# Kernel optimization log

Measured on AMD Instinct MI355X. Metric: run time of the kernel, lower is better.

## Reference

```python
import jax, jax.numpy as jnp
import numpy as np

B, L, H, V = 2048, 1024, 64, 64
LN_EPS = 1e-5
DELTA_EPS = 1e-6


def setup_inputs() -> dict:
    key = jax.random.key(0)
    ks = jax.random.split(key, 16)
    s = 0.05
    return {
        'seq': jax.random.randint(ks[0], (B, L), 0, V),
        'embed_W': jax.random.normal(ks[1], (V, H), jnp.float32),
        'ff_w1': jax.random.normal(ks[2], (H, 2 * H), jnp.float32) * s,
        'ff_b1': jnp.zeros((2 * H,), jnp.float32),
        'ff_w2': jax.random.normal(ks[3], (2 * H, H), jnp.float32) * s,
        'ff_b2': jnp.zeros((H,), jnp.float32),
        'ln_g': jnp.ones((H,), jnp.float32),
        'ln_b': jnp.zeros((H,), jnp.float32),
        'gate_w1': jax.random.normal(ks[4], (H, 16), jnp.float32) * s,
        'gate_b1': jnp.zeros((16,), jnp.float32),
        'gate_w2': jax.random.normal(ks[5], (16, 1), jnp.float32) * s,
        'gate_b2': jnp.zeros((1,), jnp.float32),
        'read_w': jax.random.normal(ks[6], (H, H), jnp.float32) * s,
        'read_b': jnp.zeros((H,), jnp.float32),
        'out_w': jax.random.normal(ks[7], (H, V), jnp.float32) * s,
        'out_b': jnp.zeros((V,), jnp.float32),
    }


def _layernorm(x, g, b):
    mu = jnp.mean(x, axis=-1, keepdims=True)
    var = jnp.var(x, axis=-1, keepdims=True)
    return (x - mu) * jax.lax.rsqrt(var + LN_EPS) * g + b


def reference(seq, embed_W, ff_w1, ff_b1, ff_w2, ff_b2, ln_g, ln_b,
              gate_w1, gate_b1, gate_w2, gate_b2, read_w, read_b, out_w, out_b):
    h = embed_W[seq]                                        # (B, L, H)
    ff = jnp.maximum(h @ ff_w1 + ff_b1, 0.0) @ ff_w2 + ff_b2
    h = _layernorm(h + ff, ln_g, ln_b)                      # (B, L, H)

    ks_seq = jnp.transpose(h[:, :-1, :], (1, 0, 2))         # (L-1, B, H) keys for scan

    def step(M, k):
        # k: (B, H); M: (B, H, H) fast-weight memory
        g = jax.nn.sigmoid(jnp.maximum(k @ gate_w1 + gate_b1, 0.0) @ gate_w2 + gate_b2)  # (B, 1)
        v_pred = jnp.einsum('bij,bj->bi', jax.lax.stop_gradient(M), k)
        denom = jnp.sum(k * k, axis=-1, keepdims=True) + DELTA_EPS
        dv = k - v_pred / denom                             # (B, H)
        dM = dv[:, :, None] * k[:, None, :]                 # outer product (B, H, H)
        return M + g[:, :, None] * dM, None

    M0 = jnp.zeros((h.shape[0], H, H), h.dtype)
    M, _ = jax.lax.scan(step, M0, ks_seq)

    q = h[:, -1, :]
    ctx = jnp.einsum('bij,bj->bi', M, q)                    # (B, H)
    logits = (ctx @ read_w + read_b) @ out_w + out_b        # (B, V)
    return logits
```

## Files before the change

### kernel.cpp

```cpp
#include <hip/hip_runtime.h>
#include <math.h>

#define Bsz 2048
#define Lsz 1024
#define SW  8

#define OFF_G   0
#define OFF_GC  4096
#define OFF_P   8192
#define OFF_WC  12288
#define OFF_GV  16384
#define OFF_C   16448
#define OFF_BC  16512

__device__ __forceinline__ float __rlf(float v, int i) {
    return __int_as_float(__builtin_amdgcn_readlane(__float_as_int(v), i));
}

__global__ __launch_bounds__(128) void prep1_kernel(
    const float* __restrict__ embed_W, const float* __restrict__ ff_w1, const float* __restrict__ ff_b1,
    const float* __restrict__ ff_w2, const float* __restrict__ ff_b2, const float* __restrict__ ln_g,
    const float* __restrict__ ln_b, const float* __restrict__ gate_w1, const float* __restrict__ gate_b1,
    const float* __restrict__ gate_w2, const float* __restrict__ gate_b2, const float* __restrict__ read_w,
    const float* __restrict__ read_b, const float* __restrict__ out_w, const float* __restrict__ out_b,
    float* __restrict__ ws)
{
    const int tid = threadIdx.x;
    const int blk = blockIdx.x;
    if (blk < 64) {
        const int v = blk;
        __shared__ float z[128];
        __shared__ float hsh[64];
        const float* Ev = embed_W + (v << 6);
        float a = ff_b1[tid];
        #pragma unroll
        for (int i = 0; i < 64; ++i) a = fmaf(Ev[i], ff_w1[i * 128 + tid], a);
        z[tid] = fmaxf(a, 0.0f);
        __syncthreads();
        if (tid < 64) {
            float x = Ev[tid] + ff_b2[tid];
            #pragma unroll
            for (int j = 0; j < 128; ++j) x = fmaf(z[j], ff_w2[j * 64 + tid], x);
            float mu = x;
            #pragma unroll
            for (int off = 32; off > 0; off >>= 1) mu += __shfl_xor(mu, off);
            mu *= (1.0f / 64.0f);
            const float dd = x - mu;
            float var = dd * dd;
            #pragma unroll
            for (int off = 32; off > 0; off >>= 1) var += __shfl_xor(var, off);
            var *= (1.0f / 64.0f);
            const float rstd = rsqrtf(var + 1e-5f);
            const float hv = fmaf(dd * rstd, ln_g[tid], ln_b[tid]);
            hsh[tid] = hv;
            float dn = hv * hv;
            #pragma unroll
            for (int off = 32; off > 0; off >>= 1) dn += __shfl_xor(dn, off);
            dn += 1e-6f;
            float a2 = 0.0f;
            if (tid < 16) {
                float um = gate_b1[tid];
                #pragma unroll
                for (int i = 0; i < 64; ++i) um = fmaf(hsh[i], gate_w1[i * 16 + tid], um);
                a2 = fmaxf(um, 0.0f) * gate_w2[tid];
            }
            #pragma unroll
            for (int off = 8; off > 0; off >>= 1) a2 += __shfl_xor(a2, off);
            ws[OFF_G + (v << 6) + tid] = hv;
            if (tid == 0) {
                a2 += gate_b2[0];
                const float g = 1.0f / (1.0f + expf(-a2));
                ws[OFF_GV + v] = g;
                ws[OFF_C + v]  = g / dn;
            }
        }
    } else if (blk < 128) {
        const int j = blk - 64;
        if (tid < 64) {
            float a = 0.0f;
            #pragma unroll
            for (int m = 0; m < 64; ++m) a = fmaf(read_w[(j << 6) + m], out_w[(m << 6) + tid], a);
            ws[OFF_WC + (j << 6) + tid] = a;
        }
    } else {
        if (tid < 64) {
            float a = out_b[tid];
            #pragma unroll
            for (int jj = 0; jj < 64; ++jj) a = fmaf(read_b[jj], out_w[(jj << 6) + tid], a);
            ws[OFF_BC + tid] = a;
        }
    }
}

__global__ __launch_bounds__(64) void prep2_kernel(float* __restrict__ ws)
{
    const int tid = threadIdx.x;
    const int blk = blockIdx.x;
    __shared__ float tT[65 * 64];
    for (int idx = tid; idx < 4096; idx += 64) {
        const int w = idx >> 6, j = idx & 63;
        tT[j * 65 + w] = ws[OFF_G + idx];
    }
    __syncthreads();
    if (blk < 64) {
        const int v = blk;
        const float cv = ws[OFF_C + v];
        float a = 0.0f;
        #pragma unroll
        for (int j = 0; j < 64; ++j) a = fmaf(tT[j * 65 + v], tT[j * 65 + tid], a);
        ws[OFF_G  + (v << 6) + tid] = a;
        ws[OFF_GC + (v << 6) + tid] = cv * a;
    } else {
        const int v = blk - 64;
        const float gv = ws[OFF_GV + v];
        float a = 0.0f;
        #pragma unroll
        for (int j = 0; j < 64; ++j)
            a = fmaf(tT[j * 65 + v], ws[OFF_WC + (j << 6) + tid], a);
        ws[OFF_P + (v << 6) + tid] = gv * a;
    }
}

__global__ __launch_bounds__(SW * 64) void scan_kernel(const int* __restrict__ seq,
                                                       const float* __restrict__ ws,
                                                       float* __restrict__ out)
{
    __shared__ float2 ldsGP[65 * 64];
    __shared__ int    pk[SW][16 + 256 + 64];
    __shared__ float  ldsbc[64];

    const int tid  = threadIdx.x;
    const int wave = tid >> 6;
    const int lane = tid & 63;

    {
        const float4* srcGc = (const float4*)(ws + OFF_GC);
        const float4* srcP  = (const float4*)(ws + OFF_P);
        for (int i = tid; i < 1024; i += SW * 64) {
            const float4 g4 = srcGc[i];
            const float4 p4 = srcP[i];
            const int base = i << 2;
            ldsGP[base + 0] = make_float2(g4.x, p4.x);
            ldsGP[base + 1] = make_float2(g4.y, p4.y);
            ldsGP[base + 2] = make_float2(g4.z, p4.z);
            ldsGP[base + 3] = make_float2(g4.w, p4.w);
        }
    }
    if (tid < 64) {
        ldsGP[4096 + tid] = make_float2(0.0f, 0.0f);
        ldsbc[tid] = ws[OFF_BC + tid];
    }
    const int b = blockIdx.x * SW + wave;
    int* P = pk[wave] + 16;
    {
        const int4* src = (const int4*)(seq + (size_t)b * Lsz);
        #pragma unroll
        for (int i = 0; i < 4; ++i) {
            const int4 tv = src[i * 64 + lane];
            P[i * 64 + lane] = tv.x | (tv.y << 8) | (tv.z << 16) | (tv.w << 24);
        }
        if (lane < 16) pk[wave][lane] = 0x40404040;
    }
    __syncthreads();

    const int lastw = P[255];
    const int tokL  = (lastw >> 24) & 0xFF;
    if (lane == 0) P[255] = (lastw & 0x00FFFFFF) | (64 << 24);

    float D   = ws[OFF_G + (tokL << 6) + lane];
    float acc = ldsbc[lane];

    int    tkA[16], tkB[16];
    float2 gpA[16], gpB[16];

    int tokv = P[248 + lane];
    #pragma unroll
    for (int j = 0; j < 4; ++j) {
        const int w = __builtin_amdgcn_readlane(tokv, 7 - j);
        tkA[4 * j + 0] = (w >> 24) & 0xFF;
        tkA[4 * j + 1] = (w >> 16) & 0xFF;
        tkA[4 * j + 2] = (w >>  8) & 0xFF;
        tkA[4 * j + 3] =  w        & 0xFF;
    }
    #pragma unroll
    for (int k = 0; k < 16; ++k) gpA[k] = ldsGP[(tkA[k] << 6) + lane];
    #pragma unroll
    for (int j = 0; j < 4; ++j) {
        const int w = __builtin_amdgcn_readlane(tokv, 3 - j);
        tkB[4 * j + 0] = (w >> 24) & 0xFF;
        tkB[4 * j + 1] = (w >> 16) & 0xFF;
        tkB[4 * j + 2] = (w >>  8) & 0xFF;
        tkB[4 * j + 3] =  w        & 0xFF;
    }
    #pragma unroll
    for (int k = 0; k < 16; ++k) gpB[k] = ldsGP[(tkB[k] << 6) + lane];

    for (int n = 0; n < 32; ++n) {
        const int tokvN = P[240 - 8 * n + lane];
        __builtin_amdgcn_s_setprio(1);
        #pragma unroll
        for (int k = 0; k < 16; ++k) {
            const float d = __rlf(D, tkA[k]);
            D   = fmaf(-d, gpA[k].x, D);
            acc = fmaf( d, gpA[k].y, acc);
        }
        __builtin_amdgcn_s_setprio(0);
        #pragma unroll
        for (int j = 0; j < 4; ++j) {
            const int w = __builtin_amdgcn_readlane(tokvN, 7 - j);
            tkA[4 * j + 0] = (w >> 24) & 0xFF;
            tkA[4 * j + 1] = (w >> 16) & 0xFF;
            tkA[4 * j + 2] = (w >>  8) & 0xFF;
            tkA[4 * j + 3] =  w        & 0xFF;
        }
        #pragma unroll
        for (int k = 0; k < 16; ++k) gpA[k] = ldsGP[(tkA[k] << 6) + lane];
        __builtin_amdgcn_s_setprio(1);
        #pragma unroll
        for (int k = 0; k < 16; ++k) {
            const float d = __rlf(D, tkB[k]);
            D   = fmaf(-d, gpB[k].x, D);
            acc = fmaf( d, gpB[k].y, acc);
        }
        __builtin_amdgcn_s_setprio(0);
        #pragma unroll
        for (int j = 0; j < 4; ++j) {
            const int w = __builtin_amdgcn_readlane(tokvN, 3 - j);
            tkB[4 * j + 0] = (w >> 24) & 0xFF;
            tkB[4 * j + 1] = (w >> 16) & 0xFF;
            tkB[4 * j + 2] = (w >>  8) & 0xFF;
            tkB[4 * j + 3] =  w        & 0xFF;
        }
        #pragma unroll
        for (int k = 0; k < 16; ++k) gpB[k] = ldsGP[(tkB[k] << 6) + lane];
    }

    out[(size_t)b * 64 + lane] = acc;
}

extern "C" void kernel_launch(void* const* d_in, const int* in_sizes, int n_in,
                              void* d_out, int out_size, void* d_ws, size_t ws_size,
                              hipStream_t stream) {
    const int*   seq     = (const int*)  d_in[0];
    const float* embed_W = (const float*)d_in[1];
    const float* ff_w1   = (const float*)d_in[2];
    const float* ff_b1   = (const float*)d_in[3];
    const float* ff_w2   = (const float*)d_in[4];
    const float* ff_b2   = (const float*)d_in[5];
    const float* ln_g    = (const float*)d_in[6];
    const float* ln_b    = (const float*)d_in[7];
    const float* gate_w1 = (const float*)d_in[8];
    const float* gate_b1 = (const float*)d_in[9];
    const float* gate_w2 = (const float*)d_in[10];
    const float* gate_b2 = (const float*)d_in[11];
    const float* read_w  = (const float*)d_in[12];
    const float* read_b  = (const float*)d_in[13];
    const float* out_w   = (const float*)d_in[14];
    const float* out_b   = (const float*)d_in[15];
    float* ws  = (float*)d_ws;
    float* out = (float*)d_out;

    hipLaunchKernelGGL(prep1_kernel, dim3(129), dim3(128), 0, stream,
                       embed_W, ff_w1, ff_b1, ff_w2, ff_b2, ln_g, ln_b,
                       gate_w1, gate_b1, gate_w2, gate_b2, read_w, read_b,
                       out_w, out_b, ws);
    hipLaunchKernelGGL(prep2_kernel, dim3(128), dim3(64), 0, stream, ws);
    hipLaunchKernelGGL(scan_kernel, dim3(Bsz / SW), dim3(SW * 64), 0, stream,
                       seq, ws, out);
}
```

Baseline: 121.5 us.

## Block the serial scan recurrence into 4-step triangular solves to shorten dependency chain

Replaces the strictly sequential per-token update (readlane of D, then two FMAs) with blocks of four tokens. For each block, all four D values are read up front, a small lower-triangular system is solved using cross-token Gram entries fetched via readlane, and then D and acc are updated. This is meant to shorten the serial readlane-to-FMA dependency chain, which limits latency in a single-wave scan. The cost is more readlanes and FMAs per token, plus some floating-point reassociation.

```diff
diff --git a/kernel.cpp b/kernel.cpp
--- a/kernel.cpp
+++ b/kernel.cpp
@@ -121,6 +121,37 @@
     }
 }
 
+#define SUB4(tk, gp, q)                                                          \
+  {                                                                              \
+    const int   t0 = tk[4*(q)+0], t1 = tk[4*(q)+1], t2 = tk[4*(q)+2], t3 = tk[4*(q)+3]; \
+    const float2 g0 = gp[4*(q)+0], g1 = gp[4*(q)+1], g2 = gp[4*(q)+2], g3 = gp[4*(q)+3]; \
+    const float M10 = __rlf(g0.x, t1);                                           \
+    const float M20 = __rlf(g0.x, t2);                                           \
+    const float M21 = __rlf(g1.x, t2);                                           \
+    const float M30 = __rlf(g0.x, t3);                                           \
+    const float M31 = __rlf(g1.x, t3);                                           \
+    const float M32 = __rlf(g2.x, t3);                                           \
+    const float b0 = __rlf(D, t0);                                               \
+    const float b1 = __rlf(D, t1);                                               \
+    const float b2 = __rlf(D, t2);                                               \
+    const float b3 = __rlf(D, t3);                                               \
+    const float d0 = b0;                                                         \
+    const float d1 = fmaf(-M10, d0, b1);                                         \
+    const float p2 = fmaf(-M20, d0, b2);                                         \
+    const float d2 = fmaf(-M21, d1, p2);                                         \
+    const float p3 = fmaf(-M30, d0, b3);                                         \
+    const float q3 = fmaf(-M31, d1, p3);                                         \
+    const float d3 = fmaf(-M32, d2, q3);                                         \
+    D = fmaf(-d0, g0.x, D);                                                      \
+    D = fmaf(-d1, g1.x, D);                                                      \
+    D = fmaf(-d2, g2.x, D);                                                      \
+    D = fmaf(-d3, g3.x, D);                                                      \
+    acc = fmaf(d0, g0.y, acc);                                                   \
+    acc = fmaf(d1, g1.y, acc);                                                   \
+    acc = fmaf(d2, g2.y, acc);                                                   \
+    acc = fmaf(d3, g3.y, acc);                                                   \
+  }
+
 __global__ __launch_bounds__(SW * 64) void scan_kernel(const int* __restrict__ seq,
                                                        const float* __restrict__ ws,
                                                        float* __restrict__ out)
@@ -198,12 +229,10 @@
     for (int n = 0; n < 32; ++n) {
         const int tokvN = P[240 - 8 * n + lane];
         __builtin_amdgcn_s_setprio(1);
-        #pragma unroll
-        for (int k = 0; k < 16; ++k) {
-            const float d = __rlf(D, tkA[k]);
-            D   = fmaf(-d, gpA[k].x, D);
-            acc = fmaf( d, gpA[k].y, acc);
-        }
+        SUB4(tkA, gpA, 0)
+        SUB4(tkA, gpA, 1)
+        SUB4(tkA, gpA, 2)
+        SUB4(tkA, gpA, 3)
         __builtin_amdgcn_s_setprio(0);
         #pragma unroll
         for (int j = 0; j < 4; ++j) {
@@ -216,12 +245,10 @@
         #pragma unroll
         for (int k = 0; k < 16; ++k) gpA[k] = ldsGP[(tkA[k] << 6) + lane];
         __builtin_amdgcn_s_setprio(1);
-        #pragma unroll
-        for (int k = 0; k < 16; ++k) {
-            const float d = __rlf(D, tkB[k]);
-            D   = fmaf(-d, gpB[k].x, D);
-            acc = fmaf( d, gpB[k].y, acc);
-        }
+        SUB4(tkB, gpB, 0)
+        SUB4(tkB, gpB, 1)
+        SUB4(tkB, gpB, 2)
+        SUB4(tkB, gpB, 3)
         __builtin_amdgcn_s_setprio(0);
         #pragma unroll
         for (int j = 0; j < 4; ++j) {
```

New measurement: 139.8 us. +15.0%, slower.
